# Kernel tuning notes

Hardware: AMD Instinct MI355X
Metric: run time of the kernel (lower is better)

Reference implementation:

```python
import jax, jax.numpy as jnp
import numpy as np

M_RANGE = 2
N_CLASS = 25
IM_CHANNEL = 3


def _conv(x, kernel, pad):
    # torch F.conv2d (cross-correlation), NCHW / OIHW, stride 1, symmetric padding
    return jax.lax.conv_general_dilated(
        x, kernel, window_strides=(1, 1),
        padding=[(pad, pad), (pad, pad)],
        dimension_numbers=('NCHW', 'OIHW', 'NCHW'))


def _label2mask(motion, n_class):
    # motion: [B,1,H,W] int labels -> one-hot mask [B,n_class,H,W]
    oh = jax.nn.one_hot(motion[:, 0], n_class, dtype=jnp.float32)  # [B,H,W,K]
    return jnp.transpose(oh, (0, 3, 1, 2))


def _construct_image(im, m_mask, appear, kernel, pad):
    # im: [B,C,H,W], m_mask: [B,K,H,W], appear: [B,1,H,W]
    im = im * appear
    B, C, H, W = im.shape
    K = m_mask.shape[1]
    # fuse the per-channel / per-sample torch loops into one batched conv
    x = (im[:, :, None] * m_mask[:, None]).reshape(B * C, K, H, W)
    return _conv(x, kernel, pad).reshape(B, C, H, W)


def setup_inputs() -> dict:
    key = jax.random.key(0)
    k1, k2, k3, k4, k5 = jax.random.split(key, 5)
    B, H, W = 32, 192, 192
    return {
        'im_input_f': jax.random.normal(k1, (B, 6, H, W), dtype=jnp.float32),
        'im_input_b': jax.random.normal(k2, (B, 6, H, W), dtype=jnp.float32),
        'gt_motion_f': jax.random.randint(k3, (B, 1, H, W), 0, N_CLASS, dtype=jnp.int64),
        'gt_motion_b': jax.random.randint(k4, (B, 1, H, W), 0, N_CLASS, dtype=jnp.int64),
        'm_kernel': jax.random.uniform(k5, (1, N_CLASS, 2 * M_RANGE + 1, 2 * M_RANGE + 1), dtype=jnp.float32),
    }


def reference(im_input_f, im_input_b, gt_motion_f, gt_motion_b, m_kernel):
    mask_f = _label2mask(gt_motion_f, N_CLASS)
    mask_b = _label2mask(gt_motion_b, N_CLASS)
    seg_f = _conv(mask_f, m_kernel, M_RANGE)  # [B,1,H,W]
    seg_b = _conv(mask_b, m_kernel, M_RANGE)
    appear_f = jax.nn.relu(1.0 - jax.nn.relu(seg_f - 1.0))
    appear_b = jax.nn.relu(1.0 - jax.nn.relu(seg_b - 1.0))
    pred_f = _construct_image(im_input_f[:, -IM_CHANNEL:], mask_f, appear_f, m_kernel, M_RANGE)
    pred_b = _construct_image(im_input_b[:, -IM_CHANNEL:], mask_b, appear_b, m_kernel, M_RANGE)
    seg_f = 1.0 - jax.nn.relu(1.0 - seg_f)
    seg_b = 1.0 - jax.nn.relu(1.0 - seg_b)
    attn = (seg_f + 1e-5) / (seg_f + seg_b + 2e-5)
    pred = attn * pred_f + (1.0 - attn) * pred_b
    return (pred, mask_f, 1.0 - appear_f, attn, mask_b, 1.0 - appear_b, 1.0 - attn)
```

## Files before the change

### kernel.cpp

```cpp
#include <hip/hip_runtime.h>

typedef float f32x4 __attribute__((ext_vector_type(4)));

namespace {
constexpr int BATCH = 32;
constexpr int H = 192;
constexpr int W = 192;
constexpr int HW = H * W;
constexpr int NCLS = 25;
constexpr int LUTN = 26 * 25;

constexpr int OFF_PRED   = 0;
constexpr int OFF_MASKF  = BATCH * 3 * HW;
constexpr int OFF_OMAF   = OFF_MASKF + BATCH * NCLS * HW;
constexpr int OFF_ATTN   = OFF_OMAF + BATCH * HW;
constexpr int OFF_MASKB  = OFF_ATTN + BATCH * HW;
constexpr int OFF_OMAB   = OFF_MASKB + BATCH * NCLS * HW;
constexpr int OFF_OMATTN = OFF_OMAB + BATCH * HW;

constexpr int TY = 8;
constexpr int SROWS = TY + 4;
constexpr int SW = W + 8;
constexpr int GPR = W / 4;
constexpr int NTHR = GPR * TY;
constexpr int YT = H / TY;
constexpr int NBLK = BATCH * YT;
constexpr float SENT = 2.0f * NCLS;
}

__device__ __forceinline__ void nt_store4(float* p, float a, float b, float c, float d) {
    f32x4 v = {a, b, c, d};
    __builtin_nontemporal_store(v, reinterpret_cast<f32x4*>(p));
}

__device__ __forceinline__ void lab_win12(int lw[12], const int* __restrict__ row, int xabs) {
    if (xabs >= 4) {
        const int4 a = *reinterpret_cast<const int4*>(row + xabs - 4);
        lw[0] = a.x; lw[1] = a.y; lw[2] = a.z; lw[3] = a.w;
    } else {
        lw[0] = NCLS; lw[1] = NCLS; lw[2] = NCLS; lw[3] = NCLS;
    }
    {
        const int4 c = *reinterpret_cast<const int4*>(row + xabs);
        lw[4] = c.x; lw[5] = c.y; lw[6] = c.z; lw[7] = c.w;
    }
    if (xabs <= W - 8) {
        const int4 e = *reinterpret_cast<const int4*>(row + xabs + 4);
        lw[8] = e.x; lw[9] = e.y; lw[10] = e.z; lw[11] = e.w;
    } else {
        lw[8] = NCLS; lw[9] = NCLS; lw[10] = NCLS; lw[11] = NCLS;
    }
}

__device__ __forceinline__ void f4_win12(float w[12], const float* __restrict__ row, int xabs) {
    if (xabs >= 4) {
        const float4 a = *reinterpret_cast<const float4*>(row + xabs - 4);
        w[0] = a.x; w[1] = a.y; w[2] = a.z; w[3] = a.w;
    } else {
        w[0] = 0.f; w[1] = 0.f; w[2] = 0.f; w[3] = 0.f;
    }
    {
        const float4 c = *reinterpret_cast<const float4*>(row + xabs);
        w[4] = c.x; w[5] = c.y; w[6] = c.z; w[7] = c.w;
    }
    if (xabs <= W - 8) {
        const float4 e = *reinterpret_cast<const float4*>(row + xabs + 4);
        w[8] = e.x; w[9] = e.y; w[10] = e.z; w[11] = e.w;
    } else {
        w[8] = 0.f; w[9] = 0.f; w[10] = 0.f; w[11] = 0.f;
    }
}

template <bool INTERIOR>
__device__ __forceinline__ void stage_unit(
    int row, int g, int b, int y0,
    const int* __restrict__ labF, const int* __restrict__ labB,
    const float* __restrict__ sk,
    float (*pF)[SW], float (*pB)[SW],
    float* __restrict__ out, float at_out[4], int lf_out[4], int lb_out[4])
{
    const int yabs = y0 + row - 2;
    const int xabs = 4 * g;
    f32x4 pf = {SENT, SENT, SENT, SENT};
    f32x4 pb = pf;

    if (yabs >= 0 && yabs < H) {
        float segf[4] = {0.f, 0.f, 0.f, 0.f};
        float segb[4] = {0.f, 0.f, 0.f, 0.f};
        int lfa[4], lba[4];
        for (int dy = 0; dy < 5; ++dy) {
            const int yy = yabs + dy - 2;
            if (yy < 0 || yy >= H) continue;
            int lwF[12], lwB[12];
            lab_win12(lwF, labF + b * HW + yy * W, xabs);
            lab_win12(lwB, labB + b * HW + yy * W, xabs);
            if (dy == 2) {
#pragma unroll
                for (int i = 0; i < 4; ++i) { lfa[i] = lwF[4 + i]; lba[i] = lwB[4 + i]; }
            }
#pragma unroll
            for (int dx = 0; dx < 5; ++dx) {
                const int base = (dy * 5 + dx) * 26;
#pragma unroll
                for (int i = 0; i < 4; ++i) {
                    segf[i] += sk[base + lwF[i + dx + 2]];
                    segb[i] += sk[base + lwB[i + dx + 2]];
                }
            }
        }
        float af[4], ab[4];
#pragma unroll
        for (int i = 0; i < 4; ++i) {
            af[i] = fmaxf(1.f - fmaxf(segf[i] - 1.f, 0.f), 0.f);
            ab[i] = fmaxf(1.f - fmaxf(segb[i] - 1.f, 0.f), 0.f);
            pf[i] = 2.f * (float)lfa[i] + af[i];
            pb[i] = 2.f * (float)lba[i] + ab[i];
        }
        if (INTERIOR) {
            const int pix = b * HW + yabs * W + xabs;
            float at[4];
#pragma unroll
            for (int i = 0; i < 4; ++i) {
                const float scf = 1.f - fmaxf(1.f - segf[i], 0.f);
                const float scb = 1.f - fmaxf(1.f - segb[i], 0.f);
                at[i] = (scf + 1e-5f) / (scf + scb + 2e-5f);
                at_out[i] = at[i];
                lf_out[i] = lfa[i];
                lb_out[i] = lba[i];
            }
            nt_store4(out + OFF_OMAF + pix, 1.f - af[0], 1.f - af[1], 1.f - af[2], 1.f - af[3]);
            nt_store4(out + OFF_OMAB + pix, 1.f - ab[0], 1.f - ab[1], 1.f - ab[2], 1.f - ab[3]);
            nt_store4(out + OFF_ATTN + pix, at[0], at[1], at[2], at[3]);
            nt_store4(out + OFF_OMATTN + pix, 1.f - at[0], 1.f - at[1], 1.f - at[2], 1.f - at[3]);
        }
    }
    *reinterpret_cast<f32x4*>(&pF[row][4 + 4 * g]) = pf;
    *reinterpret_cast<f32x4*>(&pB[row][4 + 4 * g]) = pb;
}

__device__ __forceinline__ void conv_img(
    const float (*P)[SW], const float* __restrict__ im,
    const float* __restrict__ sk, const int lab4[4],
    float* __restrict__ mbase,
    int b, int y, int x, int r_i, int g_i, float acc[3][4])
{
    for (int dy = 0; dy < 5; ++dy) {
        const int yy = y + dy - 2;
        const bool rowok = (yy >= 0 && yy < H);

        float pw[12], v0[12], v1[12], v2[12];
        if (rowok) {
            const int srow = r_i + dy;
            *reinterpret_cast<f32x4*>(&pw[0]) =
                *reinterpret_cast<const f32x4*>(&P[srow][4 * g_i]);
            *reinterpret_cast<f32x4*>(&pw[4]) =
                *reinterpret_cast<const f32x4*>(&P[srow][4 * g_i + 4]);
            *reinterpret_cast<f32x4*>(&pw[8]) =
                *reinterpret_cast<const f32x4*>(&P[srow][4 * g_i + 8]);
            const int imo = b * (6 * HW) + 3 * HW + yy * W;
            f4_win12(v0, im + imo, x);
            f4_win12(v1, im + imo + HW, x);
            f4_win12(v2, im + imo + 2 * HW, x);
        }

#pragma unroll
        for (int kk = 0; kk < 5; ++kk) {
            const int k = dy * 5 + kk;
            nt_store4(mbase + k * HW, lab4[0] == k ? 1.f : 0.f, lab4[1] == k ? 1.f : 0.f,
                      lab4[2] == k ? 1.f : 0.f, lab4[3] == k ? 1.f : 0.f);
        }

        if (rowok) {
            int lw[12];
            float aw[12];
#pragma unroll
            for (int j = 2; j < 10; ++j) {
                const int l = (int)(pw[j] * 0.5f);
                lw[j] = l;
                aw[j] = pw[j] - 2.f * (float)l;
            }
#pragma unroll
            for (int dx = 0; dx < 5; ++dx) {
                const int base = (dy * 5 + dx) * 26;
#pragma unroll
                for (int i = 0; i < 4; ++i) {
                    const int li = i + dx + 2;
                    const float w = aw[li] * sk[base + lw[li]];
                    acc[0][i] = fmaf(w, v0[li], acc[0][i]);
                    acc[1][i] = fmaf(w, v1[li], acc[1][i]);
                    acc[2][i] = fmaf(w, v2[li], acc[2][i]);
                }
            }
        }
    }
}

__global__ __launch_bounds__(NTHR) void k_fused(
    const float* __restrict__ imF, const float* __restrict__ imB,
    const int* __restrict__ labF, const int* __restrict__ labB,
    const float* __restrict__ mk, float* __restrict__ out)
{
    __shared__ float sk[LUTN];
    __shared__ float pF[SROWS][SW];
    __shared__ float pB[SROWS][SW];

    for (int i = threadIdx.x; i < LUTN; i += NTHR) {
        const int tap = i / 26;
        const int l = i - tap * 26;
        sk[i] = (l < NCLS) ? mk[l * 25 + tap] : 0.0f;
    }
    __syncthreads();

    const int blk = blockIdx.x;
    const int by = blk % YT;
    const int b  = blk / YT;
    const int y0 = by * TY;
    const int t = threadIdx.x;
    const int r_i = t / GPR;
    const int g_i = t % GPR;

    float my_at[4];
    int lfa[4], lba[4];
    stage_unit<true>(r_i + 2, g_i, b, y0, labF, labB, sk, pF, pB, out, my_at, lfa, lba);
    if (t < 4 * GPR) {
        const int hr = t / GPR;
        const int row = (hr < 2) ? hr : hr + TY;
        float da[4]; int d1[4], d2[4];
        stage_unit<false>(row, t % GPR, b, y0, labF, labB, sk, pF, pB, out, da, d1, d2);
    } else if (t < 4 * GPR + 48) {
        const int h = t - 4 * GPR;
        const int arr = h & 1, side = (h >> 1) & 1, row = h >> 2;
        f32x4 s = {SENT, SENT, SENT, SENT};
        float* dst = arr ? &pB[row][side ? W + 4 : 0] : &pF[row][side ? W + 4 : 0];
        *reinterpret_cast<f32x4*>(dst) = s;
    }
    __syncthreads();

    const int y = y0 + r_i;
    const int x = 4 * g_i;
    const int pix = b * HW + y * W + x;

    float accF[3][4] = {};
    float accB[3][4] = {};
    conv_img(pF, imF, sk, lfa, out + OFF_MASKF + b * (NCLS * HW) + y * W + x,
             b, y, x, r_i, g_i, accF);
    conv_img(pB, imB, sk, lba, out + OFF_MASKB + b * (NCLS * HW) + y * W + x,
             b, y, x, r_i, g_i, accB);

    float* pout = out + OFF_PRED + b * (3 * HW) + y * W + x;
#pragma unroll
    for (int c = 0; c < 3; ++c) {
        float p[4];
#pragma unroll
        for (int i = 0; i < 4; ++i)
            p[i] = my_at[i] * accF[c][i] + (1.f - my_at[i]) * accB[c][i];
        nt_store4(pout + c * HW, p[0], p[1], p[2], p[3]);
    }
}

extern "C" void kernel_launch(void* const* d_in, const int* in_sizes, int n_in,
                              void* d_out, int out_size, void* d_ws, size_t ws_size,
                              hipStream_t stream) {
    const float* imF  = (const float*)d_in[0];
    const float* imB  = (const float*)d_in[1];
    const int*   labF = (const int*)d_in[2];
    const int*   labB = (const int*)d_in[3];
    const float* mk   = (const float*)d_in[4];
    float* out = (float*)d_out;

    k_fused<<<NBLK, NTHR, 0, stream>>>(imF, imB, labF, labB, mk, out);
}
```

Before: 69.48 us.

## Balance halo-row segmentation across all threads and move mask_f stores before barrier

Halo-row segmentation work was previously done by only the first 4*GPR threads, each handling 4 pixels. It is now spread over all threads at 2 pixels each, so the pre-barrier phase is better balanced. The forward one-hot mask stores are issued during the interior segmentation loop, before the barrier, to overlap them with compute. The __syncthreads is replaced by a manual lgkmcnt wait plus s_barrier, which avoids waiting on outstanding global stores at the barrier. This adds more redundant label loads for the halo and depends on hand-placed scheduling barriers being correct.

```diff
diff --git a/kernel.cpp b/kernel.cpp
--- a/kernel.cpp
+++ b/kernel.cpp
@@ -1,6 +1,7 @@
 #include <hip/hip_runtime.h>
 
 typedef float f32x4 __attribute__((ext_vector_type(4)));
+typedef float f32x2 __attribute__((ext_vector_type(2)));
 
 namespace {
 constexpr int BATCH = 32;
@@ -33,111 +34,45 @@
     __builtin_nontemporal_store(v, reinterpret_cast<f32x4*>(p));
 }
 
-__device__ __forceinline__ void lab_win12(int lw[12], const int* __restrict__ row, int xabs) {
-    if (xabs >= 4) {
-        const int4 a = *reinterpret_cast<const int4*>(row + xabs - 4);
+__device__ __forceinline__ void lab_win12(int lw[12], const int* __restrict__ row, int xb) {
+    if (xb >= 4) {
+        const int4 a = *reinterpret_cast<const int4*>(row + xb - 4);
         lw[0] = a.x; lw[1] = a.y; lw[2] = a.z; lw[3] = a.w;
     } else {
         lw[0] = NCLS; lw[1] = NCLS; lw[2] = NCLS; lw[3] = NCLS;
     }
     {
-        const int4 c = *reinterpret_cast<const int4*>(row + xabs);
+        const int4 c = *reinterpret_cast<const int4*>(row + xb);
         lw[4] = c.x; lw[5] = c.y; lw[6] = c.z; lw[7] = c.w;
     }
-    if (xabs <= W - 8) {
-        const int4 e = *reinterpret_cast<const int4*>(row + xabs + 4);
+    if (xb <= W - 8) {
+        const int4 e = *reinterpret_cast<const int4*>(row + xb + 4);
         lw[8] = e.x; lw[9] = e.y; lw[10] = e.z; lw[11] = e.w;
     } else {
         lw[8] = NCLS; lw[9] = NCLS; lw[10] = NCLS; lw[11] = NCLS;
     }
 }
 
-__device__ __forceinline__ void f4_win12(float w[12], const float* __restrict__ row, int xabs) {
-    if (xabs >= 4) {
-        const float4 a = *reinterpret_cast<const float4*>(row + xabs - 4);
+__device__ __forceinline__ void f4_win12(float w[12], const float* __restrict__ row, int xb) {
+    if (xb >= 4) {
+        const float4 a = *reinterpret_cast<const float4*>(row + xb - 4);
         w[0] = a.x; w[1] = a.y; w[2] = a.z; w[3] = a.w;
     } else {
         w[0] = 0.f; w[1] = 0.f; w[2] = 0.f; w[3] = 0.f;
     }
     {
-        const float4 c = *reinterpret_cast<const float4*>(row + xabs);
+        const float4 c = *reinterpret_cast<const float4*>(row + xb);
         w[4] = c.x; w[5] = c.y; w[6] = c.z; w[7] = c.w;
     }
-    if (xabs <= W - 8) {
-        const float4 e = *reinterpret_cast<const float4*>(row + xabs + 4);
+    if (xb <= W - 8) {
+        const float4 e = *reinterpret_cast<const float4*>(row + xb + 4);
         w[8] = e.x; w[9] = e.y; w[10] = e.z; w[11] = e.w;
     } else {
         w[8] = 0.f; w[9] = 0.f; w[10] = 0.f; w[11] = 0.f;
     }
 }
 
-template <bool INTERIOR>
-__device__ __forceinline__ void stage_unit(
-    int row, int g, int b, int y0,
-    const int* __restrict__ labF, const int* __restrict__ labB,
-    const float* __restrict__ sk,
-    float (*pF)[SW], float (*pB)[SW],
-    float* __restrict__ out, float at_out[4], int lf_out[4], int lb_out[4])
-{
-    const int yabs = y0 + row - 2;
-    const int xabs = 4 * g;
-    f32x4 pf = {SENT, SENT, SENT, SENT};
-    f32x4 pb = pf;
-
-    if (yabs >= 0 && yabs < H) {
-        float segf[4] = {0.f, 0.f, 0.f, 0.f};
-        float segb[4] = {0.f, 0.f, 0.f, 0.f};
-        int lfa[4], lba[4];
-        for (int dy = 0; dy < 5; ++dy) {
-            const int yy = yabs + dy - 2;
-            if (yy < 0 || yy >= H) continue;
-            int lwF[12], lwB[12];
-            lab_win12(lwF, labF + b * HW + yy * W, xabs);
-            lab_win12(lwB, labB + b * HW + yy * W, xabs);
-            if (dy == 2) {
-#pragma unroll
-                for (int i = 0; i < 4; ++i) { lfa[i] = lwF[4 + i]; lba[i] = lwB[4 + i]; }
-            }
-#pragma unroll
-            for (int dx = 0; dx < 5; ++dx) {
-                const int base = (dy * 5 + dx) * 26;
-#pragma unroll
-                for (int i = 0; i < 4; ++i) {
-                    segf[i] += sk[base + lwF[i + dx + 2]];
-                    segb[i] += sk[base + lwB[i + dx + 2]];
-                }
-            }
-        }
-        float af[4], ab[4];
-#pragma unroll
-        for (int i = 0; i < 4; ++i) {
-            af[i] = fmaxf(1.f - fmaxf(segf[i] - 1.f, 0.f), 0.f);
-            ab[i] = fmaxf(1.f - fmaxf(segb[i] - 1.f, 0.f), 0.f);
-            pf[i] = 2.f * (float)lfa[i] + af[i];
-            pb[i] = 2.f * (float)lba[i] + ab[i];
-        }
-        if (INTERIOR) {
-            const int pix = b * HW + yabs * W + xabs;
-            float at[4];
-#pragma unroll
-            for (int i = 0; i < 4; ++i) {
-                const float scf = 1.f - fmaxf(1.f - segf[i], 0.f);
-                const float scb = 1.f - fmaxf(1.f - segb[i], 0.f);
-                at[i] = (scf + 1e-5f) / (scf + scb + 2e-5f);
-                at_out[i] = at[i];
-                lf_out[i] = lfa[i];
-                lb_out[i] = lba[i];
-            }
-            nt_store4(out + OFF_OMAF + pix, 1.f - af[0], 1.f - af[1], 1.f - af[2], 1.f - af[3]);
-            nt_store4(out + OFF_OMAB + pix, 1.f - ab[0], 1.f - ab[1], 1.f - ab[2], 1.f - ab[3]);
-            nt_store4(out + OFF_ATTN + pix, at[0], at[1], at[2], at[3]);
-            nt_store4(out + OFF_OMATTN + pix, 1.f - at[0], 1.f - at[1], 1.f - at[2], 1.f - at[3]);
-        }
-    }
-    *reinterpret_cast<f32x4*>(&pF[row][4 + 4 * g]) = pf;
-    *reinterpret_cast<f32x4*>(&pB[row][4 + 4 * g]) = pb;
-}
-
+template <bool STORES>
 __device__ __forceinline__ void conv_img(
     const float (*P)[SW], const float* __restrict__ im,
     const float* __restrict__ sk, const int lab4[4],
@@ -163,11 +98,13 @@
             f4_win12(v2, im + imo + 2 * HW, x);
         }
 
-#pragma unroll
-        for (int kk = 0; kk < 5; ++kk) {
-            const int k = dy * 5 + kk;
-            nt_store4(mbase + k * HW, lab4[0] == k ? 1.f : 0.f, lab4[1] == k ? 1.f : 0.f,
-                      lab4[2] == k ? 1.f : 0.f, lab4[3] == k ? 1.f : 0.f);
+        if (STORES) {
+#pragma unroll
+            for (int kk = 0; kk < 5; ++kk) {
+                const int k = dy * 5 + kk;
+                nt_store4(mbase + k * HW, lab4[0] == k ? 1.f : 0.f, lab4[1] == k ? 1.f : 0.f,
+                          lab4[2] == k ? 1.f : 0.f, lab4[3] == k ? 1.f : 0.f);
+            }
         }
 
         if (rowok) {
@@ -218,34 +155,131 @@
     const int t = threadIdx.x;
     const int r_i = t / GPR;
     const int g_i = t % GPR;
+    const int y = y0 + r_i;
+    const int x = 4 * g_i;
+    const int pix = b * HW + y * W + x;
+
+    const int4 lfc = *reinterpret_cast<const int4*>(labF + pix);
+    const int4 lbc = *reinterpret_cast<const int4*>(labB + pix);
+    const int lfa[4] = {lfc.x, lfc.y, lfc.z, lfc.w};
+    const int lba[4] = {lbc.x, lbc.y, lbc.z, lbc.w};
+    float* __restrict__ mfb = out + OFF_MASKF + b * (NCLS * HW) + y * W + x;
+
+    float segf[4] = {}, segb[4] = {};
+#pragma unroll
+    for (int dy = 0; dy < 5; ++dy) {
+#pragma unroll
+        for (int kk = 0; kk < 5; ++kk) {
+            const int k = dy * 5 + kk;
+            nt_store4(mfb + k * HW, lfa[0] == k ? 1.f : 0.f, lfa[1] == k ? 1.f : 0.f,
+                      lfa[2] == k ? 1.f : 0.f, lfa[3] == k ? 1.f : 0.f);
+        }
+        const int yy = y + dy - 2;
+        if (yy >= 0 && yy < H) {
+            int lwF[12], lwB[12];
+            lab_win12(lwF, labF + b * HW + yy * W, x);
+            lab_win12(lwB, labB + b * HW + yy * W, x);
+#pragma unroll
+            for (int dx = 0; dx < 5; ++dx) {
+                const int base = (dy * 5 + dx) * 26;
+#pragma unroll
+                for (int i = 0; i < 4; ++i) {
+                    segf[i] += sk[base + lwF[i + dx + 2]];
+                    segb[i] += sk[base + lwB[i + dx + 2]];
+                }
+            }
+        }
+    }
 
     float my_at[4];
-    int lfa[4], lba[4];
-    stage_unit<true>(r_i + 2, g_i, b, y0, labF, labB, sk, pF, pB, out, my_at, lfa, lba);
-    if (t < 4 * GPR) {
-        const int hr = t / GPR;
-        const int row = (hr < 2) ? hr : hr + TY;
-        float da[4]; int d1[4], d2[4];
-        stage_unit<false>(row, t % GPR, b, y0, labF, labB, sk, pF, pB, out, da, d1, d2);
-    } else if (t < 4 * GPR + 48) {
-        const int h = t - 4 * GPR;
-        const int arr = h & 1, side = (h >> 1) & 1, row = h >> 2;
+    {
+        f32x4 pf, pb;
+        float af[4], ab[4];
+#pragma unroll
+        for (int i = 0; i < 4; ++i) {
+            af[i] = fmaxf(1.f - fmaxf(segf[i] - 1.f, 0.f), 0.f);
+            ab[i] = fmaxf(1.f - fmaxf(segb[i] - 1.f, 0.f), 0.f);
+            pf[i] = 2.f * (float)lfa[i] + af[i];
+            pb[i] = 2.f * (float)lba[i] + ab[i];
+            const float scf = 1.f - fmaxf(1.f - segf[i], 0.f);
+            const float scb = 1.f - fmaxf(1.f - segb[i], 0.f);
+            my_at[i] = (scf + 1e-5f) / (scf + scb + 2e-5f);
+        }
+        *reinterpret_cast<f32x4*>(&pF[r_i + 2][4 + x]) = pf;
+        *reinterpret_cast<f32x4*>(&pB[r_i + 2][4 + x]) = pb;
+        nt_store4(out + OFF_OMAF + pix, 1.f - af[0], 1.f - af[1], 1.f - af[2], 1.f - af[3]);
+        nt_store4(out + OFF_OMAB + pix, 1.f - ab[0], 1.f - ab[1], 1.f - ab[2], 1.f - ab[3]);
+        nt_store4(out + OFF_ATTN + pix, my_at[0], my_at[1], my_at[2], my_at[3]);
+        nt_store4(out + OFF_OMATTN + pix, 1.f - my_at[0], 1.f - my_at[1], 1.f - my_at[2],
+                  1.f - my_at[3]);
+    }
+
+    {
+        const int hrow = t / 96;
+        const int row = (hrow < 2) ? hrow : hrow + TY;
+        const int hg = t % 96;
+        const int xabs = 2 * hg;
+        const int xb = xabs & ~3;
+        const int off = (hg & 1) * 2;
+        const int yabs = y0 + row - 2;
+        f32x2 pf2 = {SENT, SENT};
+        f32x2 pb2 = {SENT, SENT};
+        if (yabs >= 0 && yabs < H) {
+            float sf[2] = {0.f, 0.f}, sb[2] = {0.f, 0.f};
+            int lf2[2], lb2[2];
+            for (int dy = 0; dy < 5; ++dy) {
+                const int yy = yabs + dy - 2;
+                if (yy < 0 || yy >= H) continue;
+                int lwF[12], lwB[12];
+                lab_win12(lwF, labF + b * HW + yy * W, xb);
+                lab_win12(lwB, labB + b * HW + yy * W, xb);
+                if (dy == 2) {
+#pragma unroll
+                    for (int i = 0; i < 2; ++i) {
+                        lf2[i] = lwF[4 + off + i];
+                        lb2[i] = lwB[4 + off + i];
+                    }
+                }
+#pragma unroll
+                for (int dx = 0; dx < 5; ++dx) {
+                    const int base = (dy * 5 + dx) * 26;
+#pragma unroll
+                    for (int i = 0; i < 2; ++i) {
+                        sf[i] += sk[base + lwF[2 + off + i + dx]];
+                        sb[i] += sk[base + lwB[2 + off + i + dx]];
+                    }
+                }
+            }
+#pragma unroll
+            for (int i = 0; i < 2; ++i) {
+                const float af = fmaxf(1.f - fmaxf(sf[i] - 1.f, 0.f), 0.f);
+                const float ab = fmaxf(1.f - fmaxf(sb[i] - 1.f, 0.f), 0.f);
+                pf2[i] = 2.f * (float)lf2[i] + af;
+                pb2[i] = 2.f * (float)lb2[i] + ab;
+            }
+        }
+        *reinterpret_cast<f32x2*>(&pF[row][4 + xabs]) = pf2;
+        *reinterpret_cast<f32x2*>(&pB[row][4 + xabs]) = pb2;
+    }
+
+    if (t < 48) {
+        const int arr = t & 1, side = (t >> 1) & 1, row = t >> 2;
         f32x4 s = {SENT, SENT, SENT, SENT};
         float* dst = arr ? &pB[row][side ? W + 4 : 0] : &pF[row][side ? W + 4 : 0];
         *reinterpret_cast<f32x4*>(dst) = s;
     }
-    __syncthreads();
-
-    const int y = y0 + r_i;
-    const int x = 4 * g_i;
-    const int pix = b * HW + y * W + x;
+
+    __builtin_amdgcn_sched_barrier(0);
+    asm volatile("s_waitcnt lgkmcnt(0)" ::: "memory");
+    __builtin_amdgcn_s_barrier();
+    __builtin_amdgcn_sched_barrier(0);
+    asm volatile("" ::: "memory");
 
     float accF[3][4] = {};
     float accB[3][4] = {};
-    conv_img(pF, imF, sk, lfa, out + OFF_MASKF + b * (NCLS * HW) + y * W + x,
-             b, y, x, r_i, g_i, accF);
-    conv_img(pB, imB, sk, lba, out + OFF_MASKB + b * (NCLS * HW) + y * W + x,
-             b, y, x, r_i, g_i, accB);
+    conv_img<false>(pF, imF, sk, lfa, nullptr, b, y, x, r_i, g_i, accF);
+    conv_img<true>(pB, imB, sk, lba, out + OFF_MASKB + b * (NCLS * HW) + y * W + x,
+                   b, y, x, r_i, g_i, accB);
 
     float* pout = out + OFF_PRED + b * (3 * HW) + y * W + x;
 #pragma unroll
```

Measured after the change: 71.02 us. +2.2%, slower.
